# Performance work log

Measured on AMD Instinct MI355X. Metric: run time of the kernel, lower is better.

Reference implementation:

```python
import jax, jax.numpy as jnp
import numpy as np
from jax import lax

N_LAYERS = 30
KERNEL = 5
MU = 255.0  # quantization_channels=256 -> mu = 255
DILATIONS = [(2 ** k) % 10 for k in range(N_LAYERS)]  # 2^k mod (n_layers/n_cycles)


def causal_conv1d(x, w, b, dilation):
    # x: [B,1,T], w: [1,1,K], b: [1]; left-pad so output is causal, same length.
    pad = (w.shape[-1] - 1) * dilation
    xp = jnp.pad(x, ((0, 0), (0, 0), (pad, 0)))
    y = lax.conv_general_dilated(xp, w, window_strides=(1,), padding='VALID',
                                 rhs_dilation=(dilation,),
                                 dimension_numbers=('NCH', 'OIH', 'NCH'))
    return y + b[None, :, None]


def setup_inputs() -> dict:
    key = jax.random.key(0)
    ks = jax.random.split(key, 12)
    B, T = 8, 262144
    s = 0.2  # keep gated activations away from saturation
    return {
        'x': jax.random.normal(ks[0], (B, 1, T), dtype=jnp.float32),
        'causal_w': jax.random.normal(ks[1], (1, 1, KERNEL), jnp.float32) * s,
        'causal_b': jnp.zeros((1,), jnp.float32),
        'filter_w': jax.random.normal(ks[2], (N_LAYERS, 1, 1, KERNEL), jnp.float32) * s,
        'filter_b': jax.random.normal(ks[3], (N_LAYERS, 1), jnp.float32) * s,
        'gate_w': jax.random.normal(ks[4], (N_LAYERS, 1, 1, KERNEL), jnp.float32) * s,
        'gate_b': jax.random.normal(ks[5], (N_LAYERS, 1), jnp.float32) * s,
        'res_w': jax.random.normal(ks[6], (N_LAYERS, 1, 1, 1), jnp.float32) * s,
        'res_b': jax.random.normal(ks[7], (N_LAYERS, 1), jnp.float32) * s,
        'conv1_w': jax.random.normal(ks[8], (1, 1, 1), jnp.float32) * s,
        'conv1_b': jnp.zeros((1,), jnp.float32),
        'conv2_w': jax.random.normal(ks[9], (1, 1, 1), jnp.float32) * s,
        'conv2_b': jnp.zeros((1,), jnp.float32),
    }


def reference(x, causal_w, causal_b, filter_w, filter_b, gate_w, gate_b,
              res_w, res_b, conv1_w, conv1_b, conv2_w, conv2_b):
    h = causal_conv1d(x, causal_w, causal_b, 1)
    skip_sum = jnp.zeros_like(h)
    for k in range(N_LAYERS):  # fixed small layer loop; dilation is static per layer
        d = DILATIONS[k]
        f = jnp.tanh(causal_conv1d(h, filter_w[k], filter_b[k], d))
        g = jax.nn.sigmoid(causal_conv1d(h, gate_w[k], gate_b[k], d))
        z = f * g
        skip_sum = skip_sum + z
        # 1x1 residual conv (1 channel) = scale + bias, then residual add
        h = z * res_w[k][0, 0, 0] + res_b[k][0] + h
    out = jax.nn.relu(skip_sum) * conv1_w[0, 0, 0] + conv1_b[0]
    out = jax.nn.relu(out) * conv2_w[0, 0, 0] + conv2_b[0]
    # mu-law expanding
    out = jnp.sign(out) * (jnp.power(1.0 + MU, jnp.abs(out)) - 1.0) / MU
    return jax.nn.softmax(out, axis=-1)
```

## Files before the change

kernel.cpp:

```cpp
#include <hip/hip_runtime.h>
#include <cmath>

#define T_LEN 262144
#define NROW 8
#define NL 30
#define NT 512
#define PPT 7
#define EXT (NT * PPT)
#define HALO 576
#define TILE (EXT - HALO)
#define PB ((T_LEN + TILE - 1) / TILE)
#define PAD 32
#define CH 4096
#define RB (T_LEN / CH)
#define NB2 (NROW * RB)

#define LOG2E_2 2.885390082f
#define NLOG2E  -1.4426950409f

__device__ __forceinline__ float fast_rcp(float x) { return __builtin_amdgcn_rcpf(x); }

template<int D>
__device__ __forceinline__ void layer_step(
    int k,
    const float* __restrict__ fw, const float* __restrict__ fb,
    const float* __restrict__ gw, const float* __restrict__ gb,
    const float* __restrict__ rw, const float* __restrict__ rb,
    float* __restrict__ hb, float (&h)[PPT], float (&skip)[PPT],
    int tid, bool writeback)
{
    const float f0 = fw[k*5+0], f1 = fw[k*5+1], f2 = fw[k*5+2], f3 = fw[k*5+3], f4 = fw[k*5+4];
    const float fbk = fb[k];
    const float g0 = gw[k*5+0], g1 = gw[k*5+1], g2 = gw[k*5+2], g3 = gw[k*5+3], g4 = gw[k*5+4];
    const float gbk = gb[k];
    const float rwk = rw[k], rbk = rb[k];

    #pragma unroll
    for (int p = 0; p < PPT; ++p) {
        const int i = tid + p * NT;
        const float v0 = hb[i - 4*D];
        const float v1 = hb[i - 3*D];
        const float v2 = hb[i - 2*D];
        const float v3 = hb[i - D];
        const float v4 = h[p];

        float af = fbk;
        af = fmaf(f0, v0, af); af = fmaf(f1, v1, af); af = fmaf(f2, v2, af);
        af = fmaf(f3, v3, af); af = fmaf(f4, v4, af);
        float ag = gbk;
        ag = fmaf(g0, v0, ag); ag = fmaf(g1, v1, ag); ag = fmaf(g2, v2, ag);
        ag = fmaf(g3, v3, ag); ag = fmaf(g4, v4, ag);

        const float tf = fmaf(-2.0f, fast_rcp(exp2f(af * LOG2E_2) + 1.0f), 1.0f);
        const float sg = fast_rcp(1.0f + exp2f(ag * NLOG2E));
        const float z  = tf * sg;
        skip[p] += z;
        h[p] = fmaf(z, rwk, rbk) + v4;
    }
    if (writeback) {
        __syncthreads();
        #pragma unroll
        for (int p = 0; p < PPT; ++p) hb[tid + p * NT] = h[p];
        __syncthreads();
    }
}

__global__ __launch_bounds__(NT)
void k_wavenet(const float* __restrict__ x,
               const float* __restrict__ cw,  const float* __restrict__ cb,
               const float* __restrict__ fw,  const float* __restrict__ fb,
               const float* __restrict__ gw,  const float* __restrict__ gb,
               const float* __restrict__ rw,  const float* __restrict__ rb,
               const float* __restrict__ c1w, const float* __restrict__ c1b,
               const float* __restrict__ c2w, const float* __restrict__ c2b,
               float* __restrict__ vout, float* __restrict__ partmax)
{
    __shared__ float hraw[PAD + EXT];
    __shared__ float redm[NT / 64];
    float* hb = hraw + PAD;

    const int tid  = threadIdx.x;
    const int row  = blockIdx.x / PB;
    const int tile = blockIdx.x % PB;
    const int t0   = tile * TILE;

    if (tid < PAD) hraw[tid] = 0.0f;

    const float* xr = x + (size_t)row * T_LEN;
    float h[PPT], skip[PPT];
    #pragma unroll
    for (int p = 0; p < PPT; ++p) {
        const int i = tid + p * NT;
        const int g = t0 - HALO + i;
        const float v = (g >= 0 && g < T_LEN) ? xr[g] : 0.0f;
        hb[i] = v; h[p] = v; skip[p] = 0.0f;
    }
    __syncthreads();

    {
        const float w0 = cw[0], w1 = cw[1], w2 = cw[2], w3 = cw[3], w4 = cw[4];
        const float b  = cb[0];
        #pragma unroll
        for (int p = 0; p < PPT; ++p) {
            const int i = tid + p * NT;
            float acc = b;
            acc = fmaf(w0, hb[i-4], acc);
            acc = fmaf(w1, hb[i-3], acc);
            acc = fmaf(w2, hb[i-2], acc);
            acc = fmaf(w3, hb[i-1], acc);
            acc = fmaf(w4, h[p],    acc);
            h[p] = acc;
        }
        __syncthreads();
        #pragma unroll
        for (int p = 0; p < PPT; ++p) hb[tid + p * NT] = h[p];
        __syncthreads();
    }

    layer_step<1>(0, fw, fb, gw, gb, rw, rb, hb, h, skip, tid, true);
    int k = 1;
    #pragma unroll 1
    for (int c = 0; c < 7; ++c) {
        layer_step<2>(k+0, fw, fb, gw, gb, rw, rb, hb, h, skip, tid, true);
        layer_step<4>(k+1, fw, fb, gw, gb, rw, rb, hb, h, skip, tid, true);
        layer_step<8>(k+2, fw, fb, gw, gb, rw, rb, hb, h, skip, tid, true);
        layer_step<6>(k+3, fw, fb, gw, gb, rw, rb, hb, h, skip, tid, true);
        k += 4;
    }
    layer_step<2>(29, fw, fb, gw, gb, rw, rb, hb, h, skip, tid, false);

    const float w1 = c1w[0], b1 = c1b[0], w2 = c2w[0], b2 = c2b[0];
    float m = -INFINITY;
    float* vr = vout + (size_t)row * T_LEN;
    #pragma unroll
    for (int p = 0; p < PPT; ++p) {
        const int i = tid + p * NT;
        if (i >= HALO) {
            const int t = t0 + i - HALO;
            if (t < T_LEN) {
                float o = fmaf(fmaxf(skip[p], 0.0f), w1, b1);
                o = fmaf(fmaxf(o, 0.0f), w2, b2);
                const float a = fabsf(o);
                float v = (exp2f(8.0f * a) - 1.0f) * (1.0f / 255.0f);
                v = copysignf(v, o);
                vr[t] = v;
                m = fmaxf(m, v);
            }
        }
    }
    #pragma unroll
    for (int off = 32; off >= 1; off >>= 1)
        m = fmaxf(m, __shfl_xor(m, off, 64));
    if ((tid & 63) == 0) redm[tid >> 6] = m;
    __syncthreads();
    if (tid == 0) {
        float mm = redm[0];
        #pragma unroll
        for (int w = 1; w < NT / 64; ++w) mm = fmaxf(mm, redm[w]);
        partmax[blockIdx.x] = mm;
    }
}

__global__ __launch_bounds__(256)
void k_softmax_exp(float* __restrict__ vbuf, const float* __restrict__ partmax,
                   float* __restrict__ partsum)
{
    const int tid = threadIdx.x;
    const int row = blockIdx.x / RB;

    __shared__ float red[4];
    float m = -INFINITY;
    for (int j = tid; j < PB; j += 256) m = fmaxf(m, partmax[row * PB + j]);
    #pragma unroll
    for (int off = 32; off >= 1; off >>= 1)
        m = fmaxf(m, __shfl_xor(m, off, 64));
    if ((tid & 63) == 0) red[tid >> 6] = m;
    __syncthreads();
    const float rm = fmaxf(fmaxf(red[0], red[1]), fmaxf(red[2], red[3]));

    float4* vp = (float4*)(vbuf + (size_t)blockIdx.x * CH);
    float s = 0.0f;
    #pragma unroll
    for (int q = 0; q < 4; ++q) {
        float4 v = vp[tid + q * 256];
        v.x = __expf(v.x - rm); v.y = __expf(v.y - rm);
        v.z = __expf(v.z - rm); v.w = __expf(v.w - rm);
        s += (v.x + v.y) + (v.z + v.w);
        vp[tid + q * 256] = v;
    }
    #pragma unroll
    for (int off = 32; off >= 1; off >>= 1)
        s += __shfl_xor(s, off, 64);
    __shared__ float reds[4];
    if ((tid & 63) == 0) reds[tid >> 6] = s;
    __syncthreads();
    if (tid == 0) partsum[blockIdx.x] = (reds[0] + reds[1]) + (reds[2] + reds[3]);
}

__global__ __launch_bounds__(256)
void k_softmax_norm(float* __restrict__ vbuf, const float* __restrict__ partsum)
{
    const int tid = threadIdx.x;
    const int row = blockIdx.x / RB;

    float s = (tid < RB) ? partsum[row * RB + tid] : 0.0f;
    #pragma unroll
    for (int off = 32; off >= 1; off >>= 1)
        s += __shfl_xor(s, off, 64);
    __shared__ float sinv;
    if (tid == 0) sinv = 1.0f / s;
    __syncthreads();
    const float inv = sinv;

    float4* vp = (float4*)(vbuf + (size_t)blockIdx.x * CH);
    #pragma unroll
    for (int q = 0; q < 4; ++q) {
        float4 v = vp[tid + q * 256];
        v.x *= inv; v.y *= inv; v.z *= inv; v.w *= inv;
        vp[tid + q * 256] = v;
    }
}

extern "C" void kernel_launch(void* const* d_in, const int* in_sizes, int n_in,
                              void* d_out, int out_size, void* d_ws, size_t ws_size,
                              hipStream_t stream)
{
    const float* x   = (const float*)d_in[0];
    const float* cw  = (const float*)d_in[1];
    const float* cb  = (const float*)d_in[2];
    const float* fw  = (const float*)d_in[3];
    const float* fb  = (const float*)d_in[4];
    const float* gw  = (const float*)d_in[5];
    const float* gb  = (const float*)d_in[6];
    const float* rw  = (const float*)d_in[7];
    const float* rb  = (const float*)d_in[8];
    const float* c1w = (const float*)d_in[9];
    const float* c1b = (const float*)d_in[10];
    const float* c2w = (const float*)d_in[11];
    const float* c2b = (const float*)d_in[12];

    float* vout    = (float*)d_out;
    float* partmax = (float*)d_ws;
    float* partsum = partmax + 1024;

    k_wavenet<<<NROW * PB, NT, 0, stream>>>(x, cw, cb, fw, fb, gw, gb, rw, rb,
                                            c1w, c1b, c2w, c2b, vout, partmax);
    k_softmax_exp<<<NB2, 256, 0, stream>>>(vout, partmax, partsum);
    k_softmax_norm<<<NB2, 256, 0, stream>>>(vout, partsum);
}
```

Before: 169.8 us.

## Double-buffer layer state, fuse softmax exp into WaveNet kernel, enlarge blocks

```diff
diff --git a/kernel.cpp b/kernel.cpp
--- a/kernel.cpp
+++ b/kernel.cpp
@@ -4,8 +4,8 @@
 #define T_LEN 262144
 #define NROW 8
 #define NL 30
-#define NT 512
-#define PPT 7
+#define NT 1024
+#define PPT 3
 #define EXT (NT * PPT)
 #define HALO 576
 #define TILE (EXT - HALO)
@@ -26,8 +26,8 @@
     const float* __restrict__ fw, const float* __restrict__ fb,
     const float* __restrict__ gw, const float* __restrict__ gb,
     const float* __restrict__ rw, const float* __restrict__ rb,
-    float* __restrict__ hb, float (&h)[PPT], float (&skip)[PPT],
-    int tid, bool writeback)
+    const float* __restrict__ src, float* __restrict__ dst,
+    float (&h)[PPT], float (&skip)[PPT], int tid, bool writeback)
 {
     const float f0 = fw[k*5+0], f1 = fw[k*5+1], f2 = fw[k*5+2], f3 = fw[k*5+3], f4 = fw[k*5+4];
     const float fbk = fb[k];
@@ -38,10 +38,10 @@
     #pragma unroll
     for (int p = 0; p < PPT; ++p) {
         const int i = tid + p * NT;
-        const float v0 = hb[i - 4*D];
-        const float v1 = hb[i - 3*D];
-        const float v2 = hb[i - 2*D];
-        const float v3 = hb[i - D];
+        const float v0 = src[i - 4*D];
+        const float v1 = src[i - 3*D];
+        const float v2 = src[i - 2*D];
+        const float v3 = src[i - D];
         const float v4 = h[p];
 
         float af = fbk;
@@ -51,16 +51,15 @@
         ag = fmaf(g0, v0, ag); ag = fmaf(g1, v1, ag); ag = fmaf(g2, v2, ag);
         ag = fmaf(g3, v3, ag); ag = fmaf(g4, v4, ag);
 
-        const float tf = fmaf(-2.0f, fast_rcp(exp2f(af * LOG2E_2) + 1.0f), 1.0f);
-        const float sg = fast_rcp(1.0f + exp2f(ag * NLOG2E));
-        const float z  = tf * sg;
+        const float E1 = exp2f(af * LOG2E_2);
+        const float E2 = exp2f(ag * NLOG2E);
+        const float z  = (E1 - 1.0f) * fast_rcp((E1 + 1.0f) * (1.0f + E2));
         skip[p] += z;
         h[p] = fmaf(z, rwk, rbk) + v4;
     }
     if (writeback) {
-        __syncthreads();
-        #pragma unroll
-        for (int p = 0; p < PPT; ++p) hb[tid + p * NT] = h[p];
+        #pragma unroll
+        for (int p = 0; p < PPT; ++p) dst[tid + p * NT] = h[p];
         __syncthreads();
     }
 }
@@ -73,18 +72,20 @@
                const float* __restrict__ rw,  const float* __restrict__ rb,
                const float* __restrict__ c1w, const float* __restrict__ c1b,
                const float* __restrict__ c2w, const float* __restrict__ c2b,
-               float* __restrict__ vout, float* __restrict__ partmax)
-{
-    __shared__ float hraw[PAD + EXT];
-    __shared__ float redm[NT / 64];
-    float* hb = hraw + PAD;
+               float* __restrict__ eout, float* __restrict__ partsum)
+{
+    __shared__ float hrawA[PAD + EXT];
+    __shared__ float hrawB[PAD + EXT];
+    __shared__ float reds[NT / 64];
+    float* bufA = hrawA + PAD;
+    float* bufB = hrawB + PAD;
 
     const int tid  = threadIdx.x;
     const int row  = blockIdx.x / PB;
     const int tile = blockIdx.x % PB;
     const int t0   = tile * TILE;
 
-    if (tid < PAD) hraw[tid] = 0.0f;
+    if (tid < PAD) { hrawA[tid] = 0.0f; hrawB[tid] = 0.0f; }
 
     const float* xr = x + (size_t)row * T_LEN;
     float h[PPT], skip[PPT];
@@ -93,7 +94,7 @@
         const int i = tid + p * NT;
         const int g = t0 - HALO + i;
         const float v = (g >= 0 && g < T_LEN) ? xr[g] : 0.0f;
-        hb[i] = v; h[p] = v; skip[p] = 0.0f;
+        bufA[i] = v; h[p] = v; skip[p] = 0.0f;
     }
     __syncthreads();
 
@@ -104,34 +105,33 @@
         for (int p = 0; p < PPT; ++p) {
             const int i = tid + p * NT;
             float acc = b;
-            acc = fmaf(w0, hb[i-4], acc);
-            acc = fmaf(w1, hb[i-3], acc);
-            acc = fmaf(w2, hb[i-2], acc);
-            acc = fmaf(w3, hb[i-1], acc);
-            acc = fmaf(w4, h[p],    acc);
+            acc = fmaf(w0, bufA[i-4], acc);
+            acc = fmaf(w1, bufA[i-3], acc);
+            acc = fmaf(w2, bufA[i-2], acc);
+            acc = fmaf(w3, bufA[i-1], acc);
+            acc = fmaf(w4, h[p],      acc);
             h[p] = acc;
         }
+        #pragma unroll
+        for (int p = 0; p < PPT; ++p) bufB[tid + p * NT] = h[p];
         __syncthreads();
-        #pragma unroll
-        for (int p = 0; p < PPT; ++p) hb[tid + p * NT] = h[p];
-        __syncthreads();
-    }
-
-    layer_step<1>(0, fw, fb, gw, gb, rw, rb, hb, h, skip, tid, true);
+    }
+
+    layer_step<1>(0, fw, fb, gw, gb, rw, rb, bufB, bufA, h, skip, tid, true);
     int k = 1;
     #pragma unroll 1
     for (int c = 0; c < 7; ++c) {
-        layer_step<2>(k+0, fw, fb, gw, gb, rw, rb, hb, h, skip, tid, true);
-        layer_step<4>(k+1, fw, fb, gw, gb, rw, rb, hb, h, skip, tid, true);
-        layer_step<8>(k+2, fw, fb, gw, gb, rw, rb, hb, h, skip, tid, true);
-        layer_step<6>(k+3, fw, fb, gw, gb, rw, rb, hb, h, skip, tid, true);
+        layer_step<2>(k+0, fw, fb, gw, gb, rw, rb, bufA, bufB, h, skip, tid, true);
+        layer_step<4>(k+1, fw, fb, gw, gb, rw, rb, bufB, bufA, h, skip, tid, true);
+        layer_step<8>(k+2, fw, fb, gw, gb, rw, rb, bufA, bufB, h, skip, tid, true);
+        layer_step<6>(k+3, fw, fb, gw, gb, rw, rb, bufB, bufA, h, skip, tid, true);
         k += 4;
     }
-    layer_step<2>(29, fw, fb, gw, gb, rw, rb, hb, h, skip, tid, false);
+    layer_step<2>(29, fw, fb, gw, gb, rw, rb, bufA, bufB, h, skip, tid, false);
 
     const float w1 = c1w[0], b1 = c1b[0], w2 = c2w[0], b2 = c2b[0];
-    float m = -INFINITY;
-    float* vr = vout + (size_t)row * T_LEN;
+    float s = 0.0f;
+    float* er = eout + (size_t)row * T_LEN;
     #pragma unroll
     for (int p = 0; p < PPT; ++p) {
         const int i = tid + p * NT;
@@ -143,76 +143,43 @@
                 const float a = fabsf(o);
                 float v = (exp2f(8.0f * a) - 1.0f) * (1.0f / 255.0f);
                 v = copysignf(v, o);
-                vr[t] = v;
-                m = fmaxf(m, v);
+                const float e = __expf(v);
+                er[t] = e;
+                s += e;
             }
         }
     }
     #pragma unroll
     for (int off = 32; off >= 1; off >>= 1)
-        m = fmaxf(m, __shfl_xor(m, off, 64));
-    if ((tid & 63) == 0) redm[tid >> 6] = m;
+        s += __shfl_xor(s, off, 64);
+    if ((tid & 63) == 0) reds[tid >> 6] = s;
     __syncthreads();
     if (tid == 0) {
-        float mm = redm[0];
-        #pragma unroll
-        for (int w = 1; w < NT / 64; ++w) mm = fmaxf(mm, redm[w]);
-        partmax[blockIdx.x] = mm;
+        float ss = 0.0f;
+        #pragma unroll
+        for (int w = 0; w < NT / 64; ++w) ss += reds[w];
+        partsum[blockIdx.x] = ss;
     }
 }
 
 __global__ __launch_bounds__(256)
-void k_softmax_exp(float* __restrict__ vbuf, const float* __restrict__ partmax,
-                   float* __restrict__ partsum)
+void k_scale(float* __restrict__ ebuf, const float* __restrict__ partsum)
 {
     const int tid = threadIdx.x;
     const int row = blockIdx.x / RB;
 
     __shared__ float red[4];
-    float m = -INFINITY;
-    for (int j = tid; j < PB; j += 256) m = fmaxf(m, partmax[row * PB + j]);
-    #pragma unroll
-    for (int off = 32; off >= 1; off >>= 1)
-        m = fmaxf(m, __shfl_xor(m, off, 64));
-    if ((tid & 63) == 0) red[tid >> 6] = m;
-    __syncthreads();
-    const float rm = fmaxf(fmaxf(red[0], red[1]), fmaxf(red[2], red[3]));
-
-    float4* vp = (float4*)(vbuf + (size_t)blockIdx.x * CH);
     float s = 0.0f;
-    #pragma unroll
-    for (int q = 0; q < 4; ++q) {
-        float4 v = vp[tid + q * 256];
-        v.x = __expf(v.x - rm); v.y = __expf(v.y - rm);
-        v.z = __expf(v.z - rm); v.w = __expf(v.w - rm);
-        s += (v.x + v.y) + (v.z + v.w);
-        vp[tid + q * 256] = v;
-    }
+    for (int j = tid; j < PB; j += 256) s += partsum[row * PB + j];
     #pragma unroll
     for (int off = 32; off >= 1; off >>= 1)
         s += __shfl_xor(s, off, 64);
-    __shared__ float reds[4];
-    if ((tid & 63) == 0) reds[tid >> 6] = s;
+    if ((tid & 63) == 0) red[tid >> 6] = s;
     __syncthreads();
-    if (tid == 0) partsum[blockIdx.x] = (reds[0] + reds[1]) + (reds[2] + reds[3]);
-}
-
-__global__ __launch_bounds__(256)
-void k_softmax_norm(float* __restrict__ vbuf, const float* __restrict__ partsum)
-{
-    const int tid = threadIdx.x;
-    const int row = blockIdx.x / RB;
-
-    float s = (tid < RB) ? partsum[row * RB + tid] : 0.0f;
-    #pragma unroll
-    for (int off = 32; off >= 1; off >>= 1)
-        s += __shfl_xor(s, off, 64);
-    __shared__ float sinv;
-    if (tid == 0) sinv = 1.0f / s;
-    __syncthreads();
-    const float inv = sinv;
-
-    float4* vp = (float4*)(vbuf + (size_t)blockIdx.x * CH);
+    const float tot = (red[0] + red[1]) + (red[2] + red[3]);
+    const float inv = 1.0f / tot;
+
+    float4* vp = (float4*)(ebuf + (size_t)blockIdx.x * CH);
     #pragma unroll
     for (int q = 0; q < 4; ++q) {
         float4 v = vp[tid + q * 256];
@@ -239,12 +206,10 @@
     const float* c2w = (const float*)d_in[11];
     const float* c2b = (const float*)d_in[12];
 
-    float* vout    = (float*)d_out;
-    float* partmax = (float*)d_ws;
-    float* partsum = partmax + 1024;
+    float* eout    = (float*)d_out;
+    float* partsum = (float*)d_ws;
 
     k_wavenet<<<NROW * PB, NT, 0, stream>>>(x, cw, cb, fw, fb, gw, gb, rw, rb,
-                                            c1w, c1b, c2w, c2b, vout, partmax);
-    k_softmax_exp<<<NB2, 256, 0, stream>>>(vout, partmax, partsum);
-    k_softmax_norm<<<NB2, 256, 0, stream>>>(vout, partsum);
-}
+                                            c1w, c1b, c2w, c2b, eout, partsum);
+    k_scale<<<NB2, 256, 0, stream>>>(eout, partsum);
+}
```

After: 185.9 us. 9.5% more time.
